# Optimization experiments

Hardware: AMD Instinct MI355X
Metric: run time of the kernel (lower is better)

## Reference

```python
import jax, jax.numpy as jnp
import numpy as np

D = 128          # embedding dim
N_INIT = 100000  # number of initial (axiom) clauses
L = 64           # topological levels of derived clauses
M = 4096         # derived clauses per level
N_THAX = 2000    # distinct axiom-name (thax) embeddings
N_SINE = 32      # sine-level embeddings
N_RULES = 256    # distinct inference rules (each with its own 2-ary MLP)
N_TOT = N_INIT + L * M


def setup_inputs() -> dict:
    key = jax.random.key(0)
    ks = jax.random.split(key, 10)
    rng = np.random.default_rng(0)
    # parents of level-l nodes point to any node created strictly earlier
    parents = np.stack(
        [rng.integers(0, N_INIT + l * M, size=(M, 2)) for l in range(L)]
    ).astype(np.int32)  # [L, M, 2]
    return {
        "thax_table": jax.random.normal(ks[0], (N_THAX, D), jnp.float32) * 0.1,
        "sine_table": jax.random.normal(ks[1], (N_SINE, D), jnp.float32) * 0.1,
        "rule_W": jax.random.normal(ks[2], (N_RULES, 2 * D, D), jnp.float32) * (1.0 / np.sqrt(2 * D)),
        "rule_b": jax.random.normal(ks[3], (N_RULES, D), jnp.float32) * 0.01,
        "eval_w": jax.random.normal(ks[4], (D,), jnp.float32) * (1.0 / np.sqrt(D)),
        "eval_b": jax.random.normal(ks[5], (1,), jnp.float32) * 0.01,
        "pos_vals": jax.random.uniform(ks[6], (N_TOT,), jnp.float32, 0.01, 1.0),
        "neg_vals": jax.random.uniform(ks[7], (N_TOT,), jnp.float32, 0.01, 1.0),
        "init_thax": jax.random.randint(ks[8], (N_INIT,), 0, N_THAX, jnp.int32),
        "init_sine": jax.random.randint(ks[9], (N_INIT,), 0, N_SINE, jnp.int32),
        "parents": jnp.asarray(parents),
        "rules": jnp.asarray(rng.integers(0, N_RULES, size=(L, M)).astype(np.int32)),
    }


def reference(thax_table, sine_table, rule_W, rule_b, eval_w, eval_b,
              pos_vals, neg_vals, init_thax, init_sine, parents, rules):
    n_init = init_thax.shape[0]
    n_lvl, m = rules.shape
    d = thax_table.shape[1]

    # init nodes: embed = init_embeds[thax]() + sine_embedder(sine)
    init_emb = thax_table[init_thax] + sine_table[init_sine]  # [N_INIT, D]
    store0 = jnp.concatenate(
        [init_emb, jnp.zeros((n_lvl * m, d), init_emb.dtype)], axis=0)  # [N_TOT, D]

    # deriv nodes, level by level: gather 2 parents, per-rule MLP (cat -> Linear -> ReLU)
    def step(store, xs):
        lvl, par, rul = xs                       # par: [M,2] int, rul: [M] int
        pe = store[par].reshape(m, 2 * d)        # gather parent embeddings
        emb = jax.nn.relu(jnp.einsum('mi,mio->mo', pe, rule_W[rul]) + rule_b[rul])
        store = jax.lax.dynamic_update_slice(store, emb, (n_init + lvl * m, 0))
        return store, None

    store, _ = jax.lax.scan(step, store0, (jnp.arange(n_lvl), parents, rules))

    # eval_net + weighted BCEWithLogits (pos_weight = tot_neg / tot_pos)
    logits = store @ eval_w + eval_b[0]          # [N_TOT]
    tot = pos_vals + neg_vals
    y = pos_vals / tot
    pw = jnp.sum(neg_vals) / jnp.sum(pos_vals)
    per_node = pw * y * jax.nn.softplus(-logits) + (1.0 - y) * jax.nn.softplus(logits)
    loss = jnp.sum(tot * per_node).reshape(1)
    posOK = jnp.sum(jnp.where(logits >= 0.0, pos_vals, 0.0))
    negOK = jnp.sum(jnp.where(logits < 0.0, neg_vals, 0.0))
    return (loss, posOK, negOK)
```

## Files before the change

### kernel.cpp

```cpp
#include <hip/hip_runtime.h>

#define D      128
#define NINIT  100000
#define LVLS   64
#define M      4096
#define NRULES 256
#define NTOT   (NINIT + LVLS * M)
#define NTHR   512
#define TILE   32
#define SPLIT16 1280000

typedef __attribute__((ext_vector_type(8))) short short8;
typedef __attribute__((ext_vector_type(4))) float floatx4;

#define ST_OFF 256
#define SI_OFF (ST_OFF + (size_t)NTOT * D * 2)
#define RO_OFF (SI_OFF + (size_t)LVLS * M * 4)
#define FL_OFF (RO_OFF + (size_t)LVLS * (NRULES + 1) * 4)

#define CBAR() asm volatile("" ::: "memory")

__device__ __forceinline__ unsigned short f2bf(float x) {
  unsigned u = __float_as_uint(x);
  u += 0x7fffu + ((u >> 16) & 1u);
  return (unsigned short)(u >> 16);
}

__device__ __forceinline__ float softplusf(float x) {
  return fmaxf(x, 0.f) + log1pf(expf(-fabsf(x)));
}

__device__ __forceinline__ void st_sys(unsigned* p, unsigned v) {
  __hip_atomic_store(p, v, __ATOMIC_RELAXED, __HIP_MEMORY_SCOPE_SYSTEM);
}
__device__ __forceinline__ void st_sys64(unsigned long long* p,
                                         unsigned long long v) {
  __hip_atomic_store(p, v, __ATOMIC_RELAXED, __HIP_MEMORY_SCOPE_SYSTEM);
}
__device__ __forceinline__ unsigned ld_sys(const unsigned* p) {
  return __hip_atomic_load(p, __ATOMIC_RELAXED, __HIP_MEMORY_SCOPE_SYSTEM);
}

__device__ __forceinline__ void wait2(const unsigned* f0, bool n0,
                                      const unsigned* f1, bool n1) {
  if (__all(!(n0 || n1))) return;
  unsigned a0 = ld_sys(f0), a1 = ld_sys(f1);
  unsigned b0 = ld_sys(f0), b1 = ld_sys(f1);
  int guard = 1 << 16;
  for (;;) {
    unsigned c0 = ld_sys(f0), c1 = ld_sys(f1);
    if (__all((!n0 || a0 != 0u) && (!n1 || a1 != 0u)) || !--guard) break;
    a0 = ld_sys(f0); a1 = ld_sys(f1);
    if (__all((!n0 || b0 != 0u) && (!n1 || b1 != 0u)) || !--guard) break;
    b0 = ld_sys(f0); b1 = ld_sys(f1);
    if (__all((!n0 || c0 != 0u) && (!n1 || c1 != 0u)) || !--guard) break;
    c0 = ld_sys(f0); c1 = ld_sys(f1);
  }
  CBAR();
}

__device__ __forceinline__ void gbar_light(unsigned* bcnt, unsigned* bgen) {
  __syncthreads();
  if (threadIdx.x == 0) {
    unsigned g = ld_sys(bgen);
    unsigned v = __hip_atomic_fetch_add(bcnt, 1u, __ATOMIC_RELAXED,
                                        __HIP_MEMORY_SCOPE_SYSTEM);
    if (v == gridDim.x - 1) {
      st_sys(bcnt, 0u);
      st_sys(bgen, g + 1u);
    } else {
      int guard = 1 << 22;
      while (ld_sys(bgen) == g && --guard) __builtin_amdgcn_s_sleep(2);
    }
  }
  __syncthreads();
}

__device__ __forceinline__ bool adv_cursor(int r, const int* __restrict__ ro,
                                           int& l, int& t0, int& off, int& cnt) {
  t0 += TILE;
  while (t0 >= cnt) {
    if (++l >= LVLS) return false;
    off = ro[l * (NRULES + 1) + r];
    cnt = ro[l * (NRULES + 1) + r + 1] - off;
    t0 = 0;
  }
  return true;
}

__global__ __launch_bounds__(NTHR, 2) void fused_kernel(
    const float* __restrict__ thax_table, const float* __restrict__ sine_table,
    const float* __restrict__ rule_W, const float* __restrict__ rule_b,
    const float* __restrict__ eval_w, const float* __restrict__ eval_b,
    const float* __restrict__ pos, const float* __restrict__ neg,
    const int* __restrict__ init_thax, const int* __restrict__ init_sine,
    const int* __restrict__ parents,
    const int* __restrict__ rules,
    unsigned short* __restrict__ store, int* __restrict__ sorted_idx,
    int* __restrict__ rule_off, unsigned* __restrict__ flags,
    float* __restrict__ sums, unsigned* __restrict__ bvars,
    float* __restrict__ out) {
  __shared__ unsigned short pe[TILE * 264];
  __shared__ unsigned short ot[TILE * 136];
  __shared__ int s_sid[2][TILE];
  __shared__ int s_cnt[NRULES];
  __shared__ int s_base[NRULES + 1];
  __shared__ float racc[4];

  unsigned* bcnt = bvars;
  unsigned* bgen = bvars + 1;

  const int r = blockIdx.x;
  const int tid = threadIdx.x;
  const int wave = tid >> 6, lane = tid & 63;
  const int col = (wave << 4) + (lane & 15);
  const int node = tid >> 4;
  const int segq = tid & 15;
  const int dummyF = ((r << 3) | wave) << 4;

  float aP1 = 0.f, aP2 = 0.f, a_pos = 0.f, a_neg = 0.f;
  const float eb = eval_b[0];
  float w8[8];
  {
    float4 wA = ((const float4*)eval_w)[segq * 2];
    float4 wB = ((const float4*)eval_w)[segq * 2 + 1];
    w8[0] = wA.x; w8[1] = wA.y; w8[2] = wA.z; w8[3] = wA.w;
    w8[4] = wB.x; w8[5] = wB.y; w8[6] = wB.z; w8[7] = wB.w;
  }

  short8 bf[8];
  {
    const float* Wr = rule_W + (size_t)r * (2 * D * D);
    const int krow_base = (lane >> 4) * 8;
#pragma unroll
    for (int ks = 0; ks < 8; ++ks) {
      union { short8 s; unsigned short us[8]; } c;
#pragma unroll
      for (int j = 0; j < 8; ++j)
        c.us[j] = f2bf(Wr[(size_t)(ks * 32 + krow_base + j) * D + col]);
      bf[ks] = c.s;
    }
  }
  const float bias = rule_b[r * D + col];

  auto init_body = [&](int idx0, int hi, int stride) {
    for (int idx = idx0; idx < hi; idx += stride) {
      int nd = idx >> 4, sg = idx & 15;
      const float4* t = (const float4*)(thax_table + (size_t)init_thax[nd] * D) + sg * 2;
      const float4* s = (const float4*)(sine_table + (size_t)init_sine[nd] * D) + sg * 2;
      float4 a0 = t[0], a1 = t[1], b0 = s[0], b1 = s[1];
      float v[8] = {a0.x + b0.x, a0.y + b0.y, a0.z + b0.z, a0.w + b0.w,
                    a1.x + b1.x, a1.y + b1.y, a1.z + b1.z, a1.w + b1.w};
      unsigned p0 = (unsigned)f2bf(v[0]) | ((unsigned)f2bf(v[1]) << 16);
      unsigned p1 = (unsigned)f2bf(v[2]) | ((unsigned)f2bf(v[3]) << 16);
      unsigned p2 = (unsigned)f2bf(v[4]) | ((unsigned)f2bf(v[5]) << 16);
      unsigned p3 = (unsigned)f2bf(v[6]) | ((unsigned)f2bf(v[7]) << 16);
      unsigned long long* dst =
          (unsigned long long*)(store + (size_t)nd * D + sg * 8);
      st_sys64(dst + 0, (unsigned long long)p0 | ((unsigned long long)p1 << 32));
      st_sys64(dst + 1, (unsigned long long)p2 | ((unsigned long long)p3 << 32));

      float pd = v[0] * w8[0] + v[1] * w8[1] + v[2] * w8[2] + v[3] * w8[3] +
                 v[4] * w8[4] + v[5] * w8[5] + v[6] * w8[6] + v[7] * w8[7];
      pd += __shfl_xor(pd, 1, 64);
      pd += __shfl_xor(pd, 2, 64);
      pd += __shfl_xor(pd, 4, 64);
      pd += __shfl_xor(pd, 8, 64);
      if (sg == 0) {
        float logit = pd + eb;
        float pp = pos[nd], nn = neg[nd];
        float tot = pp + nn, y = pp / tot;
        aP1 += tot * y * softplusf(-logit);
        aP2 += tot * (1.f - y) * softplusf(logit);
        if (logit >= 0.f) a_pos += pp; else a_neg += nn;
      }
    }
  };

  if (r < LVLS) {
    const int l = r;
    const int* rl = rules + (size_t)l * M;
    if (tid < NRULES) s_cnt[tid] = 0;
    __syncthreads();
    for (int m = tid; m < M; m += NTHR) atomicAdd(&s_cnt[rl[m]], 1);
    __syncthreads();
    int c = (tid < NRULES) ? s_cnt[tid] : 0;
    if (tid < NRULES) s_base[tid] = c;
    __syncthreads();
    for (int off = 1; off < NRULES; off <<= 1) {
      int t = (tid < NRULES && tid >= off) ? s_base[tid - off] : 0;
      __syncthreads();
      if (tid < NRULES) s_base[tid] += t;
      __syncthreads();
    }
    if (tid < NRULES) {
      int ex = s_base[tid] - c;
      st_sys((unsigned*)&rule_off[(size_t)l * (NRULES + 1) + tid],
             (unsigned)ex);
      s_cnt[tid] = ex;
    }
    if (tid == 0)
      st_sys((unsigned*)&rule_off[(size_t)l * (NRULES + 1) + NRULES],
             (unsigned)M);
    __syncthreads();
    for (int m = tid; m < M; m += NTHR) {
      int p = atomicAdd(&s_cnt[rl[m]], 1);
      st_sys((unsigned*)&sorted_idx[(size_t)l * M + p], (unsigned)m);
    }
    init_body(SPLIT16 + r * NTHR + tid, NINIT * 16, LVLS * NTHR);
  } else {
    init_body((r - LVLS) * NTHR + tid, SPLIT16, (NRULES - LVLS) * NTHR);
    const int gid3 = (r - LVLS) * NTHR + tid;
    const int gstride3 = (NRULES - LVLS) * NTHR;
    float sp = 0.f, sn = 0.f;
    for (int i = gid3; i < NTOT; i += gstride3) {
      sp += pos[i];
      sn += neg[i];
    }
    for (int m = 32; m; m >>= 1) {
      sp += __shfl_xor(sp, m, 64);
      sn += __shfl_xor(sn, m, 64);
    }
    if (lane == 0) {
      atomicAdd(&sums[0], sp);
      atomicAdd(&sums[1], sn);
    }
  }

  gbar_light(bcnt, bgen);

  const float pw = sums[1] / sums[0];

  int lL = -1, t0L = 0, offL = 0, cntL = 0;

  bool validA = adv_cursor(r, rule_off, lL, t0L, offL, cntL);
  int lA = lL, t0A = t0L, cntA = cntL;
  int parA0 = 0, parA1 = 0;
  bool lateA0 = false, lateA1 = false;
  unsigned reA0 = 1u, reA1 = 1u;
  float pPosA = 0.f, pNegA = 0.f;
  uint4 gA0 = {0, 0, 0, 0}, gA1 = {0, 0, 0, 0};
  if (validA) {
    int gj = t0A + node; if (gj > cntA - 1) gj = cntA - 1;
    int sid = sorted_idx[(size_t)lA * M + offL + gj];
    parA0 = parents[((size_t)lA * M + sid) * 2 + 0];
    parA1 = parents[((size_t)lA * M + sid) * 2 + 1];
    pPosA = pos[NINIT + lA * M + sid];
    pNegA = neg[NINIT + lA * M + sid];
    bool n0 = parA0 >= NINIT, n1 = parA1 >= NINIT;
    wait2(flags + (n0 ? parA0 - NINIT : dummyF), n0,
          flags + (n1 ? parA1 - NINIT : dummyF), n1);
    gA0 = *(const uint4*)(store + (size_t)parA0 * D + segq * 8);
    gA1 = *(const uint4*)(store + (size_t)parA1 * D + segq * 8);
    if (segq == 0) s_sid[0][node] = sid;
  }

  bool validB = validA && adv_cursor(r, rule_off, lL, t0L, offL, cntL);
  int lB = lL, t0B = t0L, cntB = cntL;
  int sidB = 0, parB0 = 0, parB1 = 0;
  unsigned fB0 = 1u, fB1 = 1u;
  float pPosB = 0.f, pNegB = 0.f;
  if (validB) {
    int gj = t0B + node; if (gj > cntB - 1) gj = cntB - 1;
    sidB = sorted_idx[(size_t)lB * M + offL + gj];
    parB0 = parents[((size_t)lB * M + sidB) * 2 + 0];
    parB1 = parents[((size_t)lB * M + sidB) * 2 + 1];
    fB0 = parB0 >= NINIT ? ld_sys(flags + (parB0 - NINIT)) : 1u;
    fB1 = parB1 >= NINIT ? ld_sys(flags + (parB1 - NINIT)) : 1u;
    pPosB = pos[NINIT + lB * M + sidB];
    pNegB = neg[NINIT + lB * M + sidB];
  }

  bool validC = validB && adv_cursor(r, rule_off, lL, t0L, offL, cntL);
  int lC = lL, t0C = t0L, cntC = cntL;
  int sidC = 0, parC0 = 0, parC1 = 0;
  if (validC) {
    int gj = t0C + node; if (gj > cntC - 1) gj = cntC - 1;
    sidC = sorted_idx[(size_t)lC * M + offL + gj];
    parC0 = parents[((size_t)lC * M + sidC) * 2 + 0];
    parC1 = parents[((size_t)lC * M + sidC) * 2 + 1];
  }

  bool validE = validC && adv_cursor(r, rule_off, lL, t0L, offL, cntL);
  int lE = lL, t0E = t0L, cntE = cntL;
  int sidE = 0;
  if (validE) {
    int gj = t0E + node; if (gj > cntE - 1) gj = cntE - 1;
    sidE = sorted_idx[(size_t)lE * M + offL + gj];
  }

  bool validF = validE && adv_cursor(r, rule_off, lL, t0L, offL, cntL);
  int lF = lL, t0F = t0L, offF = offL, cntF = cntL;

  int p = 0;
  while (validA) {
    {
      bool n0 = lateA0 && (reA0 == 0u);
      bool n1 = lateA1 && (reA1 == 0u);
      wait2(flags + (lateA0 ? parA0 - NINIT : dummyF), n0,
            flags + (lateA1 ? parA1 - NINIT : dummyF), n1);
      if (lateA0) gA0 = *(const uint4*)(store + (size_t)parA0 * D + segq * 8);
      if (lateA1) gA1 = *(const uint4*)(store + (size_t)parA1 * D + segq * 8);
    }

    *(uint4*)(pe + node * 264 + segq * 8) = gA0;
    *(uint4*)(pe + node * 264 + 128 + segq * 8) = gA1;
    __syncthreads();
    if (validB && segq == 0) s_sid[p ^ 1][node] = sidB;

    floatx4 acc0 = {0.f, 0.f, 0.f, 0.f}, acc1 = {0.f, 0.f, 0.f, 0.f};
#pragma unroll
    for (int ks = 0; ks < 8; ++ks) {
      short8 a0 = *(const short8*)(pe + (lane & 15) * 264 + ks * 32 + (lane >> 4) * 8);
      short8 a1 = *(const short8*)(pe + (16 + (lane & 15)) * 264 + ks * 32 + (lane >> 4) * 8);
      acc0 = __builtin_amdgcn_mfma_f32_16x16x32_bf16(a0, bf[ks], acc0, 0, 0, 0);
      acc1 = __builtin_amdgcn_mfma_f32_16x16x32_bf16(a1, bf[ks], acc1, 0, 0, 0);
    }
#pragma unroll
    for (int reg = 0; reg < 4; ++reg) {
      int row = (lane >> 4) * 4 + reg;
      float v0 = acc0[reg] + bias;
      float v1 = acc1[reg] + bias;
      ot[row * 136 + col] = f2bf(v0 > 0.f ? v0 : 0.f);
      ot[(16 + row) * 136 + col] = f2bf(v1 > 0.f ? v1 : 0.f);
    }
    __syncthreads();

    const int n_baseA = NINIT + lA * M;
#pragma unroll
    for (int k = 0; k < 4; ++k) {
      int nd = wave + 8 * k;
      if ((t0A + nd) < cntA)
        st_sys((unsigned*)(store + (size_t)(n_baseA + s_sid[p][nd]) * D) + lane,
               *(const unsigned*)(ot + nd * 136 + lane * 2));
    }
    CBAR();

    bool lateB0 = validB && parB0 >= NINIT && fB0 == 0u;
    bool lateB1 = validB && parB1 >= NINIT && fB1 == 0u;
    const unsigned short* ga0 =
        (validB && !lateB0) ? store + (size_t)parB0 * D : store;
    const unsigned short* ga1 =
        (validB && !lateB1) ? store + (size_t)parB1 * D : store;
    uint4 gB0 = *(const uint4*)(ga0 + segq * 8);
    uint4 gB1 = *(const uint4*)(ga1 + segq * 8);
    unsigned pol0 = ld_sys(
        flags + ((validC && parC0 >= NINIT) ? parC0 - NINIT : dummyF));
    unsigned pol1 = ld_sys(
        flags + ((validC && parC1 >= NINIT) ? parC1 - NINIT : dummyF));
    int idxC = NINIT + lC * M + sidC;
    float posC = pos[validC ? idxC : 0];
    float negC = neg[validC ? idxC : 0];
    int2 prE = *(const int2*)(parents +
                (validE ? (((size_t)lE * M + sidE) * 2) : 0));
    int cF = cntF > 0 ? cntF : 1;
    int gjF = t0F + node; if (gjF > cF - 1) gjF = cF - 1; if (gjF < 0) gjF = 0;
    int sidF = sorted_idx[validF ? ((size_t)lF * M + offF + gjF) : 0];
    unsigned reB0 = ld_sys(flags + (lateB0 ? parB0 - NINIT : dummyF));
    unsigned reB1 = ld_sys(flags + (lateB1 ? parB1 - NINIT : dummyF));
    CBAR();

    {
      const uint4 u = *(const uint4*)(ot + node * 136 + segq * 8);
      float pd = __uint_as_float(u.x << 16) * w8[0] +
                 __uint_as_float(u.x & 0xffff0000u) * w8[1] +
                 __uint_as_float(u.y << 16) * w8[2] +
                 __uint_as_float(u.y & 0xffff0000u) * w8[3] +
                 __uint_as_float(u.z << 16) * w8[4] +
                 __uint_as_float(u.z & 0xffff0000u) * w8[5] +
                 __uint_as_float(u.w << 16) * w8[6] +
                 __uint_as_float(u.w & 0xffff0000u) * w8[7];
      pd += __shfl_xor(pd, 1, 64);
      pd += __shfl_xor(pd, 2, 64);
      pd += __shfl_xor(pd, 4, 64);
      pd += __shfl_xor(pd, 8, 64);
      if (segq == 0 && (t0A + node) < cntA) {
        float logit = pd + eb;
        float tot = pPosA + pNegA, y = pPosA / tot;
        aP1 += tot * y * softplusf(-logit);
        aP2 += tot * (1.f - y) * softplusf(logit);
        if (logit >= 0.f) a_pos += pPosA; else a_neg += pNegA;
      }
    }

    asm volatile("s_waitcnt vmcnt(10)" ::: "memory");
    if (lane < 4) {
      int nd = wave + 8 * lane;
      int sidw = s_sid[p][nd];
      if ((t0A + nd) < cntA) st_sys(flags + lA * M + sidw, 1u);
    }
    CBAR();

    lateA0 = lateB0; lateA1 = lateB1;
    reA0 = reB0; reA1 = reB1;
    gA0 = gB0; gA1 = gB1;
    parA0 = parB0; parA1 = parB1;
    pPosA = pPosB; pNegA = pNegB;
    lA = lB; t0A = t0B; cntA = cntB; validA = validB;

    parB0 = parC0; parB1 = parC1; sidB = sidC;
    fB0 = (validC && parC0 >= NINIT) ? pol0 : 1u;
    fB1 = (validC && parC1 >= NINIT) ? pol1 : 1u;
    pPosB = posC; pNegB = negC;
    lB = lC; t0B = t0C; cntB = cntC; validB = validC;

    parC0 = validE ? prE.x : 0; parC1 = validE ? prE.y : 0;
    sidC = sidE;
    lC = lE; t0C = t0E; cntC = cntE; validC = validE;

    sidE = sidF;
    lE = lF; t0E = t0F; cntE = cntF; validE = validF;

    validF = validF && adv_cursor(r, rule_off, lL, t0L, offL, cntL);
    lF = lL; t0F = t0L; offF = offL; cntF = cntL;
    p ^= 1;
  }

  for (int m = 32; m; m >>= 1) {
    aP1   += __shfl_xor(aP1,   m, 64);
    aP2   += __shfl_xor(aP2,   m, 64);
    a_pos += __shfl_xor(a_pos, m, 64);
    a_neg += __shfl_xor(a_neg, m, 64);
  }
  if (tid == 0) { racc[0] = 0.f; racc[1] = 0.f; racc[2] = 0.f; racc[3] = 0.f; }
  __syncthreads();
  if (lane == 0) {
    atomicAdd(&racc[0], aP1);
    atomicAdd(&racc[1], aP2);
    atomicAdd(&racc[2], a_pos);
    atomicAdd(&racc[3], a_neg);
  }
  __syncthreads();
  if (tid == 0) {
    atomicAdd(&out[0], pw * racc[0] + racc[1]);
    atomicAdd(&out[1], racc[2]);
    atomicAdd(&out[2], racc[3]);
  }
}

extern "C" void kernel_launch(void* const* d_in, const int* in_sizes, int n_in,
                              void* d_out, int out_size, void* d_ws, size_t ws_size,
                              hipStream_t stream) {
  const float* thax_table = (const float*)d_in[0];
  const float* sine_table = (const float*)d_in[1];
  const float* rule_W     = (const float*)d_in[2];
  const float* rule_b     = (const float*)d_in[3];
  const float* eval_w     = (const float*)d_in[4];
  const float* eval_b     = (const float*)d_in[5];
  const float* pos_vals   = (const float*)d_in[6];
  const float* neg_vals   = (const float*)d_in[7];
  const int*   init_thax  = (const int*)d_in[8];
  const int*   init_sine  = (const int*)d_in[9];
  const int*   parents    = (const int*)d_in[10];
  const int*   rules      = (const int*)d_in[11];

  float* out = (float*)d_out;
  char* ws = (char*)d_ws;
  float* sums = (float*)ws;
  unsigned* bvars = (unsigned*)(ws + 128);
  unsigned short* store = (unsigned short*)(ws + ST_OFF);
  int* sorted_idx = (int*)(ws + SI_OFF);
  int* rule_off   = (int*)(ws + RO_OFF);
  unsigned* flags = (unsigned*)(ws + FL_OFF);

  (void)hipMemsetAsync(d_out, 0, 3 * sizeof(float), stream);
  (void)hipMemsetAsync(d_ws, 0, 256, stream);
  (void)hipMemsetAsync(ws + FL_OFF, 0, (size_t)LVLS * M * 4, stream);

  void* args[] = {&thax_table, &sine_table, &rule_W, &rule_b, &eval_w, &eval_b,
                  &pos_vals, &neg_vals, &init_thax, &init_sine, &parents,
                  &rules, &store, &sorted_idx, &rule_off, &flags, &sums,
                  &bvars, &out};
  (void)hipLaunchCooperativeKernel((void*)fused_kernel, dim3(NRULES),
                                   dim3(NTHR), args, 0, stream);
}
```

Measured before the change: 394.4 us.

## Replace flag-ordered readiness wait with checksum-validated speculative parent loads

Producers now publish a checksum of each output row in its flag instead of a plain ready bit. That lets them drop the vmcnt wait that ordered the data stores before the flag store. Consumers load parent data and flags together and retry until the data checksum matches the flag, so there is no separate wait-then-load round trip and no late-path bookkeeping. The risks are a checksum collision accepting stale or torn data, a short retry guard that can fall through with wrong data, and the extra cost of system-scope 64-bit loads and shuffles.

```diff
diff --git a/kernel.cpp b/kernel.cpp
--- a/kernel.cpp
+++ b/kernel.cpp
@@ -40,23 +40,9 @@
 __device__ __forceinline__ unsigned ld_sys(const unsigned* p) {
   return __hip_atomic_load(p, __ATOMIC_RELAXED, __HIP_MEMORY_SCOPE_SYSTEM);
 }
-
-__device__ __forceinline__ void wait2(const unsigned* f0, bool n0,
-                                      const unsigned* f1, bool n1) {
-  if (__all(!(n0 || n1))) return;
-  unsigned a0 = ld_sys(f0), a1 = ld_sys(f1);
-  unsigned b0 = ld_sys(f0), b1 = ld_sys(f1);
-  int guard = 1 << 16;
-  for (;;) {
-    unsigned c0 = ld_sys(f0), c1 = ld_sys(f1);
-    if (__all((!n0 || a0 != 0u) && (!n1 || a1 != 0u)) || !--guard) break;
-    a0 = ld_sys(f0); a1 = ld_sys(f1);
-    if (__all((!n0 || b0 != 0u) && (!n1 || b1 != 0u)) || !--guard) break;
-    b0 = ld_sys(f0); b1 = ld_sys(f1);
-    if (__all((!n0 || c0 != 0u) && (!n1 || c1 != 0u)) || !--guard) break;
-    c0 = ld_sys(f0); c1 = ld_sys(f1);
-  }
-  CBAR();
+__device__ __forceinline__ unsigned long long ld_sys64(
+    const unsigned long long* p) {
+  return __hip_atomic_load(p, __ATOMIC_RELAXED, __HIP_MEMORY_SCOPE_SYSTEM);
 }
 
 __device__ __forceinline__ void gbar_light(unsigned* bcnt, unsigned* bgen) {
@@ -236,10 +222,9 @@
   bool validA = adv_cursor(r, rule_off, lL, t0L, offL, cntL);
   int lA = lL, t0A = t0L, cntA = cntL;
   int parA0 = 0, parA1 = 0;
-  bool lateA0 = false, lateA1 = false;
-  unsigned reA0 = 1u, reA1 = 1u;
+  unsigned fA0 = 0u, fA1 = 0u;
+  unsigned long long gA0lo = 0, gA0hi = 0, gA1lo = 0, gA1hi = 0;
   float pPosA = 0.f, pNegA = 0.f;
-  uint4 gA0 = {0, 0, 0, 0}, gA1 = {0, 0, 0, 0};
   if (validA) {
     int gj = t0A + node; if (gj > cntA - 1) gj = cntA - 1;
     int sid = sorted_idx[(size_t)lA * M + offL + gj];
@@ -247,26 +232,26 @@
     parA1 = parents[((size_t)lA * M + sid) * 2 + 1];
     pPosA = pos[NINIT + lA * M + sid];
     pNegA = neg[NINIT + lA * M + sid];
-    bool n0 = parA0 >= NINIT, n1 = parA1 >= NINIT;
-    wait2(flags + (n0 ? parA0 - NINIT : dummyF), n0,
-          flags + (n1 ? parA1 - NINIT : dummyF), n1);
-    gA0 = *(const uint4*)(store + (size_t)parA0 * D + segq * 8);
-    gA1 = *(const uint4*)(store + (size_t)parA1 * D + segq * 8);
+    fA0 = ld_sys(flags + (parA0 >= NINIT ? parA0 - NINIT : dummyF));
+    fA1 = ld_sys(flags + (parA1 >= NINIT ? parA1 - NINIT : dummyF));
+    const unsigned long long* b0 =
+        (const unsigned long long*)(store + (size_t)parA0 * D + segq * 8);
+    const unsigned long long* b1 =
+        (const unsigned long long*)(store + (size_t)parA1 * D + segq * 8);
+    gA0lo = ld_sys64(b0); gA0hi = ld_sys64(b0 + 1);
+    gA1lo = ld_sys64(b1); gA1hi = ld_sys64(b1 + 1);
     if (segq == 0) s_sid[0][node] = sid;
   }
 
   bool validB = validA && adv_cursor(r, rule_off, lL, t0L, offL, cntL);
   int lB = lL, t0B = t0L, cntB = cntL;
   int sidB = 0, parB0 = 0, parB1 = 0;
-  unsigned fB0 = 1u, fB1 = 1u;
   float pPosB = 0.f, pNegB = 0.f;
   if (validB) {
     int gj = t0B + node; if (gj > cntB - 1) gj = cntB - 1;
     sidB = sorted_idx[(size_t)lB * M + offL + gj];
     parB0 = parents[((size_t)lB * M + sidB) * 2 + 0];
     parB1 = parents[((size_t)lB * M + sidB) * 2 + 1];
-    fB0 = parB0 >= NINIT ? ld_sys(flags + (parB0 - NINIT)) : 1u;
-    fB1 = parB1 >= NINIT ? ld_sys(flags + (parB1 - NINIT)) : 1u;
     pPosB = pos[NINIT + lB * M + sidB];
     pNegB = neg[NINIT + lB * M + sidB];
   }
@@ -295,16 +280,47 @@
   int p = 0;
   while (validA) {
     {
-      bool n0 = lateA0 && (reA0 == 0u);
-      bool n1 = lateA1 && (reA1 == 0u);
-      wait2(flags + (lateA0 ? parA0 - NINIT : dummyF), n0,
-            flags + (lateA1 ? parA1 - NINIT : dummyF), n1);
-      if (lateA0) gA0 = *(const uint4*)(store + (size_t)parA0 * D + segq * 8);
-      if (lateA1) gA1 = *(const uint4*)(store + (size_t)parA1 * D + segq * 8);
-    }
-
-    *(uint4*)(pe + node * 264 + segq * 8) = gA0;
-    *(uint4*)(pe + node * 264 + 128 + segq * 8) = gA1;
+      int guard = 1 << 12;
+      for (;;) {
+        unsigned s0 = (unsigned)gA0lo + (unsigned)(gA0lo >> 32) +
+                      (unsigned)gA0hi + (unsigned)(gA0hi >> 32);
+        unsigned s1 = (unsigned)gA1lo + (unsigned)(gA1lo >> 32) +
+                      (unsigned)gA1hi + (unsigned)(gA1hi >> 32);
+#pragma unroll
+        for (int m = 1; m < 16; m <<= 1) {
+          s0 += __shfl_xor(s0, m, 64);
+          s1 += __shfl_xor(s1, m, 64);
+        }
+        bool ok0 = parA0 < NINIT ||
+                   ((fA0 >> 31) && ((s0 & 0x7fffffffu) == (fA0 & 0x7fffffffu)));
+        bool ok1 = parA1 < NINIT ||
+                   ((fA1 >> 31) && ((s1 & 0x7fffffffu) == (fA1 & 0x7fffffffu)));
+        if (__all(ok0 && ok1) || !--guard) break;
+        const unsigned long long* b0 =
+            (const unsigned long long*)(store + (size_t)parA0 * D + segq * 8);
+        const unsigned long long* b1 =
+            (const unsigned long long*)(store + (size_t)parA1 * D + segq * 8);
+        if (!ok0) {
+          fA0 = ld_sys(flags + (parA0 - NINIT));
+          gA0lo = ld_sys64(b0); gA0hi = ld_sys64(b0 + 1);
+        }
+        if (!ok1) {
+          fA1 = ld_sys(flags + (parA1 - NINIT));
+          gA1lo = ld_sys64(b1); gA1hi = ld_sys64(b1 + 1);
+        }
+      }
+      CBAR();
+    }
+
+    {
+      uint4 q0, q1;
+      q0.x = (unsigned)gA0lo; q0.y = (unsigned)(gA0lo >> 32);
+      q0.z = (unsigned)gA0hi; q0.w = (unsigned)(gA0hi >> 32);
+      q1.x = (unsigned)gA1lo; q1.y = (unsigned)(gA1lo >> 32);
+      q1.z = (unsigned)gA1hi; q1.w = (unsigned)(gA1hi >> 32);
+      *(uint4*)(pe + node * 264 + segq * 8) = q0;
+      *(uint4*)(pe + node * 264 + 128 + segq * 8) = q1;
+    }
     __syncthreads();
     if (validB && segq == 0) s_sid[p ^ 1][node] = sidB;
 
@@ -326,6 +342,33 @@
     }
     __syncthreads();
 
+    unsigned cksN;
+    {
+      const uint4 u = *(const uint4*)(ot + node * 136 + segq * 8);
+      unsigned cs = u.x + u.y + u.z + u.w;
+      float pd = __uint_as_float(u.x << 16) * w8[0] +
+                 __uint_as_float(u.x & 0xffff0000u) * w8[1] +
+                 __uint_as_float(u.y << 16) * w8[2] +
+                 __uint_as_float(u.y & 0xffff0000u) * w8[3] +
+                 __uint_as_float(u.z << 16) * w8[4] +
+                 __uint_as_float(u.z & 0xffff0000u) * w8[5] +
+                 __uint_as_float(u.w << 16) * w8[6] +
+                 __uint_as_float(u.w & 0xffff0000u) * w8[7];
+#pragma unroll
+      for (int m = 1; m < 16; m <<= 1) {
+        cs += __shfl_xor(cs, m, 64);
+        pd += __shfl_xor(pd, m, 64);
+      }
+      cksN = (cs & 0x7fffffffu) | 0x80000000u;
+      if (segq == 0 && (t0A + node) < cntA) {
+        float logit = pd + eb;
+        float tot = pPosA + pNegA, y = pPosA / tot;
+        aP1 += tot * y * softplusf(-logit);
+        aP2 += tot * (1.f - y) * softplusf(logit);
+        if (logit >= 0.f) a_pos += pPosA; else a_neg += pNegA;
+      }
+    }
+
     const int n_baseA = NINIT + lA * M;
 #pragma unroll
     for (int k = 0; k < 4; ++k) {
@@ -334,20 +377,19 @@
         st_sys((unsigned*)(store + (size_t)(n_baseA + s_sid[p][nd]) * D) + lane,
                *(const unsigned*)(ot + nd * 136 + lane * 2));
     }
+    if (segq == 0 && (t0A + node) < cntA)
+      st_sys(flags + lA * M + s_sid[p][node], cksN);
     CBAR();
 
-    bool lateB0 = validB && parB0 >= NINIT && fB0 == 0u;
-    bool lateB1 = validB && parB1 >= NINIT && fB1 == 0u;
-    const unsigned short* ga0 =
-        (validB && !lateB0) ? store + (size_t)parB0 * D : store;
-    const unsigned short* ga1 =
-        (validB && !lateB1) ? store + (size_t)parB1 * D : store;
-    uint4 gB0 = *(const uint4*)(ga0 + segq * 8);
-    uint4 gB1 = *(const uint4*)(ga1 + segq * 8);
-    unsigned pol0 = ld_sys(
-        flags + ((validC && parC0 >= NINIT) ? parC0 - NINIT : dummyF));
-    unsigned pol1 = ld_sys(
-        flags + ((validC && parC1 >= NINIT) ? parC1 - NINIT : dummyF));
+    int pb0 = validB ? parB0 : 0, pb1 = validB ? parB1 : 0;
+    unsigned fB0 = ld_sys(flags + (pb0 >= NINIT ? pb0 - NINIT : dummyF));
+    unsigned fB1 = ld_sys(flags + (pb1 >= NINIT ? pb1 - NINIT : dummyF));
+    const unsigned long long* rb0 =
+        (const unsigned long long*)(store + (size_t)pb0 * D + segq * 8);
+    const unsigned long long* rb1 =
+        (const unsigned long long*)(store + (size_t)pb1 * D + segq * 8);
+    unsigned long long gB0lo = ld_sys64(rb0), gB0hi = ld_sys64(rb0 + 1);
+    unsigned long long gB1lo = ld_sys64(rb1), gB1hi = ld_sys64(rb1 + 1);
     int idxC = NINIT + lC * M + sidC;
     float posC = pos[validC ? idxC : 0];
     float negC = neg[validC ? idxC : 0];
@@ -356,51 +398,15 @@
     int cF = cntF > 0 ? cntF : 1;
     int gjF = t0F + node; if (gjF > cF - 1) gjF = cF - 1; if (gjF < 0) gjF = 0;
     int sidF = sorted_idx[validF ? ((size_t)lF * M + offF + gjF) : 0];
-    unsigned reB0 = ld_sys(flags + (lateB0 ? parB0 - NINIT : dummyF));
-    unsigned reB1 = ld_sys(flags + (lateB1 ? parB1 - NINIT : dummyF));
     CBAR();
 
-    {
-      const uint4 u = *(const uint4*)(ot + node * 136 + segq * 8);
-      float pd = __uint_as_float(u.x << 16) * w8[0] +
-                 __uint_as_float(u.x & 0xffff0000u) * w8[1] +
-                 __uint_as_float(u.y << 16) * w8[2] +
-                 __uint_as_float(u.y & 0xffff0000u) * w8[3] +
-                 __uint_as_float(u.z << 16) * w8[4] +
-                 __uint_as_float(u.z & 0xffff0000u) * w8[5] +
-                 __uint_as_float(u.w << 16) * w8[6] +
-                 __uint_as_float(u.w & 0xffff0000u) * w8[7];
-      pd += __shfl_xor(pd, 1, 64);
-      pd += __shfl_xor(pd, 2, 64);
-      pd += __shfl_xor(pd, 4, 64);
-      pd += __shfl_xor(pd, 8, 64);
-      if (segq == 0 && (t0A + node) < cntA) {
-        float logit = pd + eb;
-        float tot = pPosA + pNegA, y = pPosA / tot;
-        aP1 += tot * y * softplusf(-logit);
-        aP2 += tot * (1.f - y) * softplusf(logit);
-        if (logit >= 0.f) a_pos += pPosA; else a_neg += pNegA;
-      }
-    }
-
-    asm volatile("s_waitcnt vmcnt(10)" ::: "memory");
-    if (lane < 4) {
-      int nd = wave + 8 * lane;
-      int sidw = s_sid[p][nd];
-      if ((t0A + nd) < cntA) st_sys(flags + lA * M + sidw, 1u);
-    }
-    CBAR();
-
-    lateA0 = lateB0; lateA1 = lateB1;
-    reA0 = reB0; reA1 = reB1;
-    gA0 = gB0; gA1 = gB1;
-    parA0 = parB0; parA1 = parB1;
+    fA0 = fB0; fA1 = fB1;
+    gA0lo = gB0lo; gA0hi = gB0hi; gA1lo = gB1lo; gA1hi = gB1hi;
+    parA0 = pb0; parA1 = pb1;
     pPosA = pPosB; pNegA = pNegB;
     lA = lB; t0A = t0B; cntA = cntB; validA = validB;
 
     parB0 = parC0; parB1 = parC1; sidB = sidC;
-    fB0 = (validC && parC0 >= NINIT) ? pol0 : 1u;
-    fB1 = (validC && parC1 >= NINIT) ? pol1 : 1u;
     pPosB = posC; pNegB = negC;
     lB = lC; t0B = t0C; cntB = cntC; validB = validC;
 
```

After: 398.7 us. Within noise of the previous version (+1.1%).

## Replace per-node dataflow flags with per-level done barrier across rule blocks

Applied to the files above, without the earlier changes.

Drops the fine-grained per-node readiness flags and the multi-stage software pipeline that prefetched parents across tiles and levels. Each rule block now processes one level's tiles in order, publishes a per-level done flag, and before starting the next level spins until all 256 rule blocks have finished the previous level, read as 64-bit words spread across lanes. This removes per-node flag traffic and polling, at the cost of a level-wide barrier that lets no block run ahead and of losing the deep prefetch overlap. Only the next level's first tile is prefetched.

```diff
diff --git a/kernel.cpp b/kernel.cpp
--- a/kernel.cpp
+++ b/kernel.cpp
@@ -13,10 +13,10 @@
 typedef __attribute__((ext_vector_type(8))) short short8;
 typedef __attribute__((ext_vector_type(4))) float floatx4;
 
-#define ST_OFF 256
+#define DN_OFF 512
+#define ST_OFF (DN_OFF + (size_t)LVLS * 256 * 4)
 #define SI_OFF (ST_OFF + (size_t)NTOT * D * 2)
 #define RO_OFF (SI_OFF + (size_t)LVLS * M * 4)
-#define FL_OFF (RO_OFF + (size_t)LVLS * (NRULES + 1) * 4)
 
 #define CBAR() asm volatile("" ::: "memory")
 
@@ -40,23 +40,9 @@
 __device__ __forceinline__ unsigned ld_sys(const unsigned* p) {
   return __hip_atomic_load(p, __ATOMIC_RELAXED, __HIP_MEMORY_SCOPE_SYSTEM);
 }
-
-__device__ __forceinline__ void wait2(const unsigned* f0, bool n0,
-                                      const unsigned* f1, bool n1) {
-  if (__all(!(n0 || n1))) return;
-  unsigned a0 = ld_sys(f0), a1 = ld_sys(f1);
-  unsigned b0 = ld_sys(f0), b1 = ld_sys(f1);
-  int guard = 1 << 16;
-  for (;;) {
-    unsigned c0 = ld_sys(f0), c1 = ld_sys(f1);
-    if (__all((!n0 || a0 != 0u) && (!n1 || a1 != 0u)) || !--guard) break;
-    a0 = ld_sys(f0); a1 = ld_sys(f1);
-    if (__all((!n0 || b0 != 0u) && (!n1 || b1 != 0u)) || !--guard) break;
-    b0 = ld_sys(f0); b1 = ld_sys(f1);
-    if (__all((!n0 || c0 != 0u) && (!n1 || c1 != 0u)) || !--guard) break;
-    c0 = ld_sys(f0); c1 = ld_sys(f1);
-  }
-  CBAR();
+__device__ __forceinline__ unsigned long long ld_sys64(
+    const unsigned long long* p) {
+  return __hip_atomic_load(p, __ATOMIC_RELAXED, __HIP_MEMORY_SCOPE_SYSTEM);
 }
 
 __device__ __forceinline__ void gbar_light(unsigned* bcnt, unsigned* bgen) {
@@ -76,18 +62,6 @@
   __syncthreads();
 }
 
-__device__ __forceinline__ bool adv_cursor(int r, const int* __restrict__ ro,
-                                           int& l, int& t0, int& off, int& cnt) {
-  t0 += TILE;
-  while (t0 >= cnt) {
-    if (++l >= LVLS) return false;
-    off = ro[l * (NRULES + 1) + r];
-    cnt = ro[l * (NRULES + 1) + r + 1] - off;
-    t0 = 0;
-  }
-  return true;
-}
-
 __global__ __launch_bounds__(NTHR, 2) void fused_kernel(
     const float* __restrict__ thax_table, const float* __restrict__ sine_table,
     const float* __restrict__ rule_W, const float* __restrict__ rule_b,
@@ -97,7 +71,7 @@
     const int* __restrict__ parents,
     const int* __restrict__ rules,
     unsigned short* __restrict__ store, int* __restrict__ sorted_idx,
-    int* __restrict__ rule_off, unsigned* __restrict__ flags,
+    int* __restrict__ rule_off, unsigned* __restrict__ done,
     float* __restrict__ sums, unsigned* __restrict__ bvars,
     float* __restrict__ out) {
   __shared__ unsigned short pe[TILE * 264];
@@ -116,7 +90,6 @@
   const int col = (wave << 4) + (lane & 15);
   const int node = tid >> 4;
   const int segq = tid & 15;
-  const int dummyF = ((r << 3) | wave) << 4;
 
   float aP1 = 0.f, aP2 = 0.f, a_pos = 0.f, a_neg = 0.f;
   const float eb = eval_b[0];
@@ -231,189 +204,165 @@
 
   const float pw = sums[1] / sums[0];
 
-  int lL = -1, t0L = 0, offL = 0, cntL = 0;
-
-  bool validA = adv_cursor(r, rule_off, lL, t0L, offL, cntL);
-  int lA = lL, t0A = t0L, cntA = cntL;
-  int parA0 = 0, parA1 = 0;
-  bool lateA0 = false, lateA1 = false;
-  unsigned reA0 = 1u, reA1 = 1u;
-  float pPosA = 0.f, pNegA = 0.f;
-  uint4 gA0 = {0, 0, 0, 0}, gA1 = {0, 0, 0, 0};
-  if (validA) {
-    int gj = t0A + node; if (gj > cntA - 1) gj = cntA - 1;
-    int sid = sorted_idx[(size_t)lA * M + offL + gj];
-    parA0 = parents[((size_t)lA * M + sid) * 2 + 0];
-    parA1 = parents[((size_t)lA * M + sid) * 2 + 1];
-    pPosA = pos[NINIT + lA * M + sid];
-    pNegA = neg[NINIT + lA * M + sid];
-    bool n0 = parA0 >= NINIT, n1 = parA1 >= NINIT;
-    wait2(flags + (n0 ? parA0 - NINIT : dummyF), n0,
-          flags + (n1 ? parA1 - NINIT : dummyF), n1);
-    gA0 = *(const uint4*)(store + (size_t)parA0 * D + segq * 8);
-    gA1 = *(const uint4*)(store + (size_t)parA1 * D + segq * 8);
-    if (segq == 0) s_sid[0][node] = sid;
-  }
-
-  bool validB = validA && adv_cursor(r, rule_off, lL, t0L, offL, cntL);
-  int lB = lL, t0B = t0L, cntB = cntL;
-  int sidB = 0, parB0 = 0, parB1 = 0;
-  unsigned fB0 = 1u, fB1 = 1u;
-  float pPosB = 0.f, pNegB = 0.f;
-  if (validB) {
-    int gj = t0B + node; if (gj > cntB - 1) gj = cntB - 1;
-    sidB = sorted_idx[(size_t)lB * M + offL + gj];
-    parB0 = parents[((size_t)lB * M + sidB) * 2 + 0];
-    parB1 = parents[((size_t)lB * M + sidB) * 2 + 1];
-    fB0 = parB0 >= NINIT ? ld_sys(flags + (parB0 - NINIT)) : 1u;
-    fB1 = parB1 >= NINIT ? ld_sys(flags + (parB1 - NINIT)) : 1u;
-    pPosB = pos[NINIT + lB * M + sidB];
-    pNegB = neg[NINIT + lB * M + sidB];
-  }
-
-  bool validC = validB && adv_cursor(r, rule_off, lL, t0L, offL, cntL);
-  int lC = lL, t0C = t0L, cntC = cntL;
-  int sidC = 0, parC0 = 0, parC1 = 0;
-  if (validC) {
-    int gj = t0C + node; if (gj > cntC - 1) gj = cntC - 1;
-    sidC = sorted_idx[(size_t)lC * M + offL + gj];
-    parC0 = parents[((size_t)lC * M + sidC) * 2 + 0];
-    parC1 = parents[((size_t)lC * M + sidC) * 2 + 1];
-  }
-
-  bool validE = validC && adv_cursor(r, rule_off, lL, t0L, offL, cntL);
-  int lE = lL, t0E = t0L, cntE = cntL;
-  int sidE = 0;
-  if (validE) {
-    int gj = t0E + node; if (gj > cntE - 1) gj = cntE - 1;
-    sidE = sorted_idx[(size_t)lE * M + offL + gj];
-  }
-
-  bool validF = validE && adv_cursor(r, rule_off, lL, t0L, offL, cntL);
-  int lF = lL, t0F = t0L, offF = offL, cntF = cntL;
-
-  int p = 0;
-  while (validA) {
-    {
-      bool n0 = lateA0 && (reA0 == 0u);
-      bool n1 = lateA1 && (reA1 == 0u);
-      wait2(flags + (lateA0 ? parA0 - NINIT : dummyF), n0,
-            flags + (lateA1 ? parA1 - NINIT : dummyF), n1);
-      if (lateA0) gA0 = *(const uint4*)(store + (size_t)parA0 * D + segq * 8);
-      if (lateA1) gA1 = *(const uint4*)(store + (size_t)parA1 * D + segq * 8);
-    }
-
-    *(uint4*)(pe + node * 264 + segq * 8) = gA0;
-    *(uint4*)(pe + node * 264 + 128 + segq * 8) = gA1;
-    __syncthreads();
-    if (validB && segq == 0) s_sid[p ^ 1][node] = sidB;
-
-    floatx4 acc0 = {0.f, 0.f, 0.f, 0.f}, acc1 = {0.f, 0.f, 0.f, 0.f};
+  int off = rule_off[r];
+  int cnt = rule_off[r + 1] - off;
+  int sid = 0, par0 = 0, par1 = 0;
+  float pP = 0.f, pN = 0.f;
+  {
+    int cc = cnt > 0 ? cnt : 1;
+    int gj = node; if (gj > cc - 1) gj = cc - 1;
+    sid = sorted_idx[off + gj];
+    par0 = parents[(size_t)sid * 2 + 0];
+    par1 = parents[(size_t)sid * 2 + 1];
+    pP = pos[NINIT + sid];
+    pN = neg[NINIT + sid];
+  }
+
+  int sp = 0;
+  for (int l = 0; l < LVLS; ++l) {
+    if (l > 0) {
+      const unsigned long long* dl =
+          (const unsigned long long*)(done + (size_t)(l - 1) * 256) + lane * 2;
+      unsigned long long a0 = ld_sys64(dl), a1 = ld_sys64(dl + 1);
+      unsigned long long b0 = ld_sys64(dl), b1 = ld_sys64(dl + 1);
+      int guard = 1 << 16;
+      for (;;) {
+        unsigned long long c0 = ld_sys64(dl), c1 = ld_sys64(dl + 1);
+        bool ok = (unsigned)a0 && (unsigned)(a0 >> 32) &&
+                  (unsigned)a1 && (unsigned)(a1 >> 32);
+        if (__all(ok) || !--guard) break;
+        a0 = ld_sys64(dl); a1 = ld_sys64(dl + 1);
+        ok = (unsigned)b0 && (unsigned)(b0 >> 32) &&
+             (unsigned)b1 && (unsigned)(b1 >> 32);
+        if (__all(ok) || !--guard) break;
+        b0 = ld_sys64(dl); b1 = ld_sys64(dl + 1);
+        ok = (unsigned)c0 && (unsigned)(c0 >> 32) &&
+             (unsigned)c1 && (unsigned)(c1 >> 32);
+        if (__all(ok) || !--guard) break;
+        c0 = ld_sys64(dl); c1 = ld_sys64(dl + 1);
+      }
+      CBAR();
+    }
+
+    const bool hasN = (l + 1 < LVLS);
+    int offN = 0, cntRawN = 0;
+    if (hasN) {
+      offN = rule_off[(size_t)(l + 1) * (NRULES + 1) + r];
+      cntRawN = rule_off[(size_t)(l + 1) * (NRULES + 1) + r + 1];
+    }
+
+    const int n_base = NINIT + l * M;
+    const int nt = (cnt + TILE - 1) / TILE;
+
+    for (int t = 0; t < nt; ++t) {
+      const int t0 = t * TILE;
+      if (t > 0) {
+        int gj = t0 + node; if (gj > cnt - 1) gj = cnt - 1;
+        sid = sorted_idx[(size_t)l * M + off + gj];
+        par0 = parents[((size_t)l * M + sid) * 2 + 0];
+        par1 = parents[((size_t)l * M + sid) * 2 + 1];
+        pP = pos[n_base + sid];
+        pN = neg[n_base + sid];
+      }
+      if (segq == 0) s_sid[sp][node] = sid;
+      {
+        uint4 g0 = *(const uint4*)(store + (size_t)par0 * D + segq * 8);
+        uint4 g1 = *(const uint4*)(store + (size_t)par1 * D + segq * 8);
+        *(uint4*)(pe + node * 264 + segq * 8) = g0;
+        *(uint4*)(pe + node * 264 + 128 + segq * 8) = g1;
+      }
+      __syncthreads();
+
+      floatx4 acc0 = {0.f, 0.f, 0.f, 0.f}, acc1 = {0.f, 0.f, 0.f, 0.f};
 #pragma unroll
-    for (int ks = 0; ks < 8; ++ks) {
-      short8 a0 = *(const short8*)(pe + (lane & 15) * 264 + ks * 32 + (lane >> 4) * 8);
-      short8 a1 = *(const short8*)(pe + (16 + (lane & 15)) * 264 + ks * 32 + (lane >> 4) * 8);
-      acc0 = __builtin_amdgcn_mfma_f32_16x16x32_bf16(a0, bf[ks], acc0, 0, 0, 0);
-      acc1 = __builtin_amdgcn_mfma_f32_16x16x32_bf16(a1, bf[ks], acc1, 0, 0, 0);
-    }
+      for (int ks = 0; ks < 8; ++ks) {
+        short8 a0 = *(const short8*)(pe + (lane & 15) * 264 + ks * 32 + (lane >> 4) * 8);
+        short8 a1 = *(const short8*)(pe + (16 + (lane & 15)) * 264 + ks * 32 + (lane >> 4) * 8);
+        acc0 = __builtin_amdgcn_mfma_f32_16x16x32_bf16(a0, bf[ks], acc0, 0, 0, 0);
+        acc1 = __builtin_amdgcn_mfma_f32_16x16x32_bf16(a1, bf[ks], acc1, 0, 0, 0);
+      }
 #pragma unroll
-    for (int reg = 0; reg < 4; ++reg) {
-      int row = (lane >> 4) * 4 + reg;
-      float v0 = acc0[reg] + bias;
-      float v1 = acc1[reg] + bias;
-      ot[row * 136 + col] = f2bf(v0 > 0.f ? v0 : 0.f);
-      ot[(16 + row) * 136 + col] = f2bf(v1 > 0.f ? v1 : 0.f);
-    }
-    __syncthreads();
-
-    const int n_baseA = NINIT + lA * M;
+      for (int reg = 0; reg < 4; ++reg) {
+        int row = (lane >> 4) * 4 + reg;
+        float v0 = acc0[reg] + bias;
+        float v1 = acc1[reg] + bias;
+        ot[row * 136 + col] = f2bf(v0 > 0.f ? v0 : 0.f);
+        ot[(16 + row) * 136 + col] = f2bf(v1 > 0.f ? v1 : 0.f);
+      }
+      __syncthreads();
+
 #pragma unroll
-    for (int k = 0; k < 4; ++k) {
-      int nd = wave + 8 * k;
-      if ((t0A + nd) < cntA)
-        st_sys((unsigned*)(store + (size_t)(n_baseA + s_sid[p][nd]) * D) + lane,
-               *(const unsigned*)(ot + nd * 136 + lane * 2));
-    }
-    CBAR();
-
-    bool lateB0 = validB && parB0 >= NINIT && fB0 == 0u;
-    bool lateB1 = validB && parB1 >= NINIT && fB1 == 0u;
-    const unsigned short* ga0 =
-        (validB && !lateB0) ? store + (size_t)parB0 * D : store;
-    const unsigned short* ga1 =
-        (validB && !lateB1) ? store + (size_t)parB1 * D : store;
-    uint4 gB0 = *(const uint4*)(ga0 + segq * 8);
-    uint4 gB1 = *(const uint4*)(ga1 + segq * 8);
-    unsigned pol0 = ld_sys(
-        flags + ((validC && parC0 >= NINIT) ? parC0 - NINIT : dummyF));
-    unsigned pol1 = ld_sys(
-        flags + ((validC && parC1 >= NINIT) ? parC1 - NINIT : dummyF));
-    int idxC = NINIT + lC * M + sidC;
-    float posC = pos[validC ? idxC : 0];
-    float negC = neg[validC ? idxC : 0];
-    int2 prE = *(const int2*)(parents +
-                (validE ? (((size_t)lE * M + sidE) * 2) : 0));
-    int cF = cntF > 0 ? cntF : 1;
-    int gjF = t0F + node; if (gjF > cF - 1) gjF = cF - 1; if (gjF < 0) gjF = 0;
-    int sidF = sorted_idx[validF ? ((size_t)lF * M + offF + gjF) : 0];
-    unsigned reB0 = ld_sys(flags + (lateB0 ? parB0 - NINIT : dummyF));
-    unsigned reB1 = ld_sys(flags + (lateB1 ? parB1 - NINIT : dummyF));
-    CBAR();
-
-    {
-      const uint4 u = *(const uint4*)(ot + node * 136 + segq * 8);
-      float pd = __uint_as_float(u.x << 16) * w8[0] +
-                 __uint_as_float(u.x & 0xffff0000u) * w8[1] +
-                 __uint_as_float(u.y << 16) * w8[2] +
-                 __uint_as_float(u.y & 0xffff0000u) * w8[3] +
-                 __uint_as_float(u.z << 16) * w8[4] +
-                 __uint_as_float(u.z & 0xffff0000u) * w8[5] +
-                 __uint_as_float(u.w << 16) * w8[6] +
-                 __uint_as_float(u.w & 0xffff0000u) * w8[7];
-      pd += __shfl_xor(pd, 1, 64);
-      pd += __shfl_xor(pd, 2, 64);
-      pd += __shfl_xor(pd, 4, 64);
-      pd += __shfl_xor(pd, 8, 64);
-      if (segq == 0 && (t0A + node) < cntA) {
-        float logit = pd + eb;
-        float tot = pPosA + pNegA, y = pPosA / tot;
-        aP1 += tot * y * softplusf(-logit);
-        aP2 += tot * (1.f - y) * softplusf(logit);
-        if (logit >= 0.f) a_pos += pPosA; else a_neg += pNegA;
-      }
-    }
-
-    asm volatile("s_waitcnt vmcnt(10)" ::: "memory");
-    if (lane < 4) {
-      int nd = wave + 8 * lane;
-      int sidw = s_sid[p][nd];
-      if ((t0A + nd) < cntA) st_sys(flags + lA * M + sidw, 1u);
-    }
-    CBAR();
-
-    lateA0 = lateB0; lateA1 = lateB1;
-    reA0 = reB0; reA1 = reB1;
-    gA0 = gB0; gA1 = gB1;
-    parA0 = parB0; parA1 = parB1;
-    pPosA = pPosB; pNegA = pNegB;
-    lA = lB; t0A = t0B; cntA = cntB; validA = validB;
-
-    parB0 = parC0; parB1 = parC1; sidB = sidC;
-    fB0 = (validC && parC0 >= NINIT) ? pol0 : 1u;
-    fB1 = (validC && parC1 >= NINIT) ? pol1 : 1u;
-    pPosB = posC; pNegB = negC;
-    lB = lC; t0B = t0C; cntB = cntC; validB = validC;
-
-    parC0 = validE ? prE.x : 0; parC1 = validE ? prE.y : 0;
-    sidC = sidE;
-    lC = lE; t0C = t0E; cntC = cntE; validC = validE;
-
-    sidE = sidF;
-    lE = lF; t0E = t0F; cntE = cntF; validE = validF;
-
-    validF = validF && adv_cursor(r, rule_off, lL, t0L, offL, cntL);
-    lF = lL; t0F = t0L; offF = offL; cntF = cntL;
-    p ^= 1;
+      for (int k = 0; k < 4; ++k) {
+        int nd = wave + 8 * k;
+        if ((t0 + nd) < cnt)
+          st_sys((unsigned*)(store + (size_t)(n_base + s_sid[sp][nd]) * D) + lane,
+                 *(const unsigned*)(ot + nd * 136 + lane * 2));
+      }
+      CBAR();
+
+      const bool lastTile = (t == nt - 1);
+      int sidN = 0;
+      if (lastTile && hasN) {
+        int cN = cntRawN - offN; int cc = cN > 0 ? cN : 1;
+        int gj = node; if (gj > cc - 1) gj = cc - 1;
+        sidN = sorted_idx[(size_t)(l + 1) * M + offN + gj];
+      }
+      CBAR();
+
+      if (lastTile) {
+        __syncthreads();
+        if (hasN && tid == 0) st_sys(done + (size_t)l * 256 + r, 1u);
+        CBAR();
+      }
+
+      {
+        const uint4 u = *(const uint4*)(ot + node * 136 + segq * 8);
+        float pd = __uint_as_float(u.x << 16) * w8[0] +
+                   __uint_as_float(u.x & 0xffff0000u) * w8[1] +
+                   __uint_as_float(u.y << 16) * w8[2] +
+                   __uint_as_float(u.y & 0xffff0000u) * w8[3] +
+                   __uint_as_float(u.z << 16) * w8[4] +
+                   __uint_as_float(u.z & 0xffff0000u) * w8[5] +
+                   __uint_as_float(u.w << 16) * w8[6] +
+                   __uint_as_float(u.w & 0xffff0000u) * w8[7];
+        pd += __shfl_xor(pd, 1, 64);
+        pd += __shfl_xor(pd, 2, 64);
+        pd += __shfl_xor(pd, 4, 64);
+        pd += __shfl_xor(pd, 8, 64);
+        if (segq == 0 && (t0 + node) < cnt) {
+          float logit = pd + eb;
+          float tot = pP + pN, y = pP / tot;
+          aP1 += tot * y * softplusf(-logit);
+          aP2 += tot * (1.f - y) * softplusf(logit);
+          if (logit >= 0.f) a_pos += pP; else a_neg += pN;
+        }
+      }
+
+      if (lastTile && hasN) {
+        int2 pr = *(const int2*)(parents + ((size_t)(l + 1) * M + sidN) * 2);
+        par0 = pr.x; par1 = pr.y;
+        pP = pos[NINIT + (l + 1) * M + sidN];
+        pN = neg[NINIT + (l + 1) * M + sidN];
+        sid = sidN;
+      }
+      sp ^= 1;
+    }
+
+    if (nt == 0) {
+      if (hasN) {
+        int cN = cntRawN - offN; int cc = cN > 0 ? cN : 1;
+        int gj = node; if (gj > cc - 1) gj = cc - 1;
+        sid = sorted_idx[(size_t)(l + 1) * M + offN + gj];
+        if (tid == 0) st_sys(done + (size_t)l * 256 + r, 1u);
+        int2 pr = *(const int2*)(parents + ((size_t)(l + 1) * M + sid) * 2);
+        par0 = pr.x; par1 = pr.y;
+        pP = pos[NINIT + (l + 1) * M + sid];
+        pN = neg[NINIT + (l + 1) * M + sid];
+      }
+    }
+
+    off = offN;
+    cnt = hasN ? (cntRawN - offN) : 0;
   }
 
   for (int m = 32; m; m >>= 1) {
@@ -458,18 +407,17 @@
   char* ws = (char*)d_ws;
   float* sums = (float*)ws;
   unsigned* bvars = (unsigned*)(ws + 128);
+  unsigned* done = (unsigned*)(ws + DN_OFF);
   unsigned short* store = (unsigned short*)(ws + ST_OFF);
   int* sorted_idx = (int*)(ws + SI_OFF);
   int* rule_off   = (int*)(ws + RO_OFF);
-  unsigned* flags = (unsigned*)(ws + FL_OFF);
 
   (void)hipMemsetAsync(d_out, 0, 3 * sizeof(float), stream);
-  (void)hipMemsetAsync(d_ws, 0, 256, stream);
-  (void)hipMemsetAsync(ws + FL_OFF, 0, (size_t)LVLS * M * 4, stream);
+  (void)hipMemsetAsync(d_ws, 0, DN_OFF + (size_t)LVLS * 256 * 4, stream);
 
   void* args[] = {&thax_table, &sine_table, &rule_W, &rule_b, &eval_w, &eval_b,
                   &pos_vals, &neg_vals, &init_thax, &init_sine, &parents,
-                  &rules, &store, &sorted_idx, &rule_off, &flags, &sums,
+                  &rules, &store, &sorted_idx, &rule_off, &done, &sums,
                   &bvars, &out};
   (void)hipLaunchCooperativeKernel((void*)fused_kernel, dim3(NRULES),
                                    dim3(NTHR), args, 0, stream);
```

Measured after the change: 505.7 us. 1.28x slower.
